# Performance work log

Hardware: AMD Instinct MI355X
Metric: run time of the kernel (lower is better)

Reference implementation:

```python
import jax, jax.numpy as jnp
import numpy as np

B, T, D = 2, 2048, 512
H = 8
DH = D // H
DECAY = 0.99
SCALE = DH ** -0.5
NEG = -1e30

_J6 = jnp.array([[0, 0, 0, 0, 0, 1], [0, 0, 0, 0, -1, 0], [0, 0, 0, 1, 0, 0],
                 [0, 0, 1, 0, 0, 0], [0, -1, 0, 0, 0, 0], [1, 0, 0, 0, 0, 0]],
                dtype=jnp.float32)
_PAIRS4 = [(0, 1), (0, 2), (0, 3), (1, 2), (1, 3), (2, 3)]


def exterior(p1, p2):
    # p1, p2: [..., 4] -> normalized Plucker line coords [..., 6]
    parts = [p1[..., i] * p2[..., j] - p1[..., j] * p2[..., i] for i, j in _PAIRS4]
    L = jnp.stack(parts, axis=-1)
    n = jnp.sqrt(jnp.sum(L * L, axis=-1, keepdims=True))
    return L / jnp.maximum(n, 1e-12)


def setup_inputs() -> dict:
    key = jax.random.key(0)
    ks = jax.random.split(key, 16)
    s = 0.02
    return {
        "x": jax.random.normal(ks[0], (B, T, D), jnp.float32),
        "qkv_w": jax.random.normal(ks[1], (3 * D, D), jnp.float32) * s,
        "qkv_b": jnp.zeros((3 * D,), jnp.float32),
        "w1_write": jax.random.normal(ks[2], (4 * H, D), jnp.float32) * s,
        "w2_write": jax.random.normal(ks[3], (4 * H, D), jnp.float32) * s,
        "w1_read": jax.random.normal(ks[4], (4 * H, D), jnp.float32) * s,
        "w2_read": jax.random.normal(ks[5], (4 * H, D), jnp.float32) * s,
        "mem_value_w": jax.random.normal(ks[6], (D, D), jnp.float32) * s,
        "mem_value_b": jnp.zeros((D,), jnp.float32),
        "mem_gate_w": jax.random.normal(ks[7], (H, D), jnp.float32) * s,
        "mem_gate_b": jnp.zeros((H,), jnp.float32),
        "mem_scale": jnp.full((H,), 0.1, jnp.float32),
        "out_w": jax.random.normal(ks[8], (D, D), jnp.float32) * s,
        "out_b": jnp.zeros((D,), jnp.float32),
    }


def reference(x, qkv_w, qkv_b, w1_write, w2_write, w1_read, w2_read,
              mem_value_w, mem_value_b, mem_gate_w, mem_gate_b, mem_scale,
              out_w, out_b):
    b, t, d = x.shape
    # --- standard causal attention (dropout in eval mode = identity) ---
    qkv = (x @ qkv_w.T + qkv_b).reshape(b, t, 3, H, DH)
    qkv = jnp.transpose(qkv, (2, 0, 3, 1, 4))  # [3,B,H,T,dh]
    q, k, v = qkv[0], qkv[1], qkv[2]
    scores = jnp.einsum('bhtd,bhsd->bhts', q, k) * SCALE
    i = jnp.arange(t)
    upper = i[:, None] < i[None, :]  # strictly upper -> masked
    scores = jnp.where(upper, NEG, scores)
    attn = jax.nn.softmax(scores, axis=-1)
    seq_out = jnp.einsum('bhts,bhsd->bhtd', attn, v)
    seq_out = jnp.transpose(seq_out, (0, 2, 1, 3)).reshape(b, t, d)
    # --- exterior-algebra Gram memory ---
    x_prev = jnp.concatenate([jnp.zeros((b, 1, d), x.dtype), x[:, :-1]], axis=1)
    w1 = (x_prev @ w1_write.T).reshape(b, t, H, 4)
    w2 = (x @ w2_write.T).reshape(b, t, H, 4)
    write_lines = exterior(w1, w2)  # [B,T,H,6]
    r1 = (x @ w1_read.T).reshape(b, t, H, 4)
    r2 = (x @ w2_read.T).reshape(b, t, H, 4)
    read_lines = exterior(r1, r2)  # [B,T,H,6]
    J_write = jnp.einsum('bthi,ij->bthj', write_lines, _J6)
    # incidence[b,h,i,j] = <read_i, J write_j>
    incidence = jnp.einsum('bihk,bjhk->bhij', read_lines, J_write)  # [B,H,T,T]
    # decay weights, strictly lower triangular (j < i); also acts as causal mask
    pos = jnp.arange(t, dtype=x.dtype)
    delta = pos[:, None] - pos[None, :]
    weights = jnp.where(delta > 0, jnp.power(jnp.asarray(DECAY, x.dtype), delta), 0.0)
    mem_score = jnp.sum((incidence * incidence) * weights[None, None], axis=-1)  # [B,H,T]
    # --- gating ---
    mem_val = x @ mem_value_w.T + mem_value_b  # [B,T,D]
    gate = jax.nn.sigmoid(x @ mem_gate_w.T + mem_gate_b)  # [B,T,H]
    mem_score_t = jnp.transpose(mem_score, (0, 2, 1))  # [B,T,H]
    gated = jax.nn.sigmoid(mem_score_t * mem_scale[None, None, :]) * gate
    gated = jnp.mean(gated, axis=-1, keepdims=True)  # [B,T,1]
    return (seq_out + gated * mem_val) @ out_w.T + out_b
```

## Files before the change

### kernel.cpp

```cpp
#include <hip/hip_runtime.h>
#include <math.h>

#define B_ 2
#define T_ 2048
#define D_ 512
#define H_ 8
#define DH_ 64
#define SCALE_ 0.125f
#define DECAY_ 0.99f

static constexpr size_t QSZ = (size_t)B_ * H_ * T_ * DH_;

typedef __bf16 bf16x8 __attribute__((ext_vector_type(8)));
typedef float f32x4 __attribute__((ext_vector_type(4)));

__device__ inline ushort f2bf(float f) {
  uint u = __float_as_uint(f);
  u += 0x7FFF + ((u >> 16) & 1);
  return (ushort)(u >> 16);
}

__device__ inline float bf2f(ushort v) {
  return __uint_as_float(((uint)v) << 16);
}

__device__ __forceinline__ void gload16(const ushort* g, ushort* l) {
  __builtin_amdgcn_global_load_lds(
      (const __attribute__((address_space(1))) void*)g,
      (__attribute__((address_space(3))) void*)l, 16, 0, 0);
}

__device__ __forceinline__ uint cvtpk(float lo, float hi) {
  uint r;
  asm("v_cvt_pk_bf16_f32 %0, %1, %2" : "=v"(r) : "v"(lo), "v"(hi));
  return r;
}

__global__ __launch_bounds__(256) void cast_bf16_kernel(
    const float* __restrict__ x, const float* __restrict__ qkvw,
    const float* __restrict__ mvw, const float* __restrict__ ow,
    const float* __restrict__ w1w, const float* __restrict__ w2w,
    const float* __restrict__ w1r, const float* __restrict__ w2r,
    const float* __restrict__ mgw, ushort* __restrict__ dst)
{
  size_t e0 = ((size_t)blockIdx.x * 256 + threadIdx.x) * 8;
  const float* src = nullptr;
  if (e0 < 2097152)      src = x + e0;
  else if (e0 < 2883584) src = qkvw + (e0 - 2097152);
  else if (e0 < 3145728) src = mvw + (e0 - 2883584);
  else if (e0 < 3276800) {
    size_t off = e0 - 3145728;
    int row = (int)(off >> 9), col = (int)(off & 511);
    if (row < 32)       src = w1w + (size_t)row * 512 + col;
    else if (row < 64)  src = w2w + (size_t)(row - 32) * 512 + col;
    else if (row < 96)  src = w1r + (size_t)(row - 64) * 512 + col;
    else if (row < 128) src = w2r + (size_t)(row - 96) * 512 + col;
    else if (row < 136) src = mgw + (size_t)(row - 128) * 512 + col;
    else src = nullptr;
  } else if (e0 < 3538944) src = ow + (e0 - 3276800);
  ushort tmp[8];
  if (src) {
    float4 a = *(const float4*)(src);
    float4 b = *(const float4*)(src + 4);
    tmp[0] = f2bf(a.x); tmp[1] = f2bf(a.y); tmp[2] = f2bf(a.z); tmp[3] = f2bf(a.w);
    tmp[4] = f2bf(b.x); tmp[5] = f2bf(b.y); tmp[6] = f2bf(b.z); tmp[7] = f2bf(b.w);
  } else {
#pragma unroll
    for (int i = 0; i < 8; i++) tmp[i] = 0;
  }
  *(uint4*)(dst + e0) = *(uint4*)tmp;
}

template<int EPI>
__global__ __launch_bounds__(256) void mfma_gemm(const ushort* __restrict__ A,
    const ushort* __restrict__ W, const float* __restrict__ bias,
    const float* __restrict__ bias2, void* __restrict__ Cout,
    ushort* __restrict__ memval16, float* __restrict__ proj, int M, int N, int K)
{
  __shared__ __align__(16) ushort As[128 * 64];
  __shared__ __align__(16) ushort Ws[64 * 64];
  const int tid = threadIdx.x;
  const int wave = tid >> 6, lane = tid & 63;
  const int col16 = lane & 15, grp = lane >> 4;
  const int wr = wave >> 1, wc = wave & 1;
  const int gx = gridDim.x;
  const int nwg = gx * gridDim.y;
  const int p = blockIdx.y * gx + blockIdx.x;
  const int wg = (p & 7) * (nwg >> 3) + (p >> 3);
  const int bm = (wg / gx) * 128, bn = (wg % gx) * 64;

  f32x4 acc[4][2] = {};
  const int lrow = lane >> 3, lcol = (lane & 7) * 8;

  for (int k0 = 0; k0 < K; k0 += 64) {
    __syncthreads();
#pragma unroll
    for (int i = 0; i < 4; i++) {
      int q = i * 4 + wave;
      gload16(A + (size_t)(bm + q * 8 + lrow) * K + k0 + lcol, &As[q * 512]);
    }
#pragma unroll
    for (int i = 0; i < 2; i++) {
      int q = i * 4 + wave;
      gload16(W + (size_t)(bn + q * 8 + lrow) * K + k0 + lcol, &Ws[q * 512]);
    }
    __syncthreads();
#pragma unroll
    for (int kk = 0; kk < 2; kk++) {
      bf16x8 a[4], b[2];
#pragma unroll
      for (int m = 0; m < 4; m++)
        a[m] = *(const bf16x8*)&As[(wr * 64 + m * 16 + col16) * 64 + kk * 32 + grp * 8];
#pragma unroll
      for (int n = 0; n < 2; n++)
        b[n] = *(const bf16x8*)&Ws[(wc * 32 + n * 16 + col16) * 64 + kk * 32 + grp * 8];
#pragma unroll
      for (int m = 0; m < 4; m++)
#pragma unroll
        for (int n = 0; n < 2; n++)
          acc[m][n] = __builtin_amdgcn_mfma_f32_16x16x32_bf16(a[m], b[n], acc[m][n], 0, 0, 0);
    }
  }

  if (EPI == 1) {
    ushort* q16 = (ushort*)Cout;
    ushort* k16 = q16 + QSZ;
    ushort* vt  = q16 + 2 * QSZ;
    const int sec = bn >> 9;
    if (sec == 2) {
#pragma unroll
      for (int n = 0; n < 2; n++) {
        int col = bn + wc * 32 + n * 16 + col16;
        float bv = bias[col];
        int h = (col >> 6) & 7, dh = col & 63;
#pragma unroll
        for (int m = 0; m < 4; m++) {
          int row0 = bm + wr * 64 + m * 16 + grp * 4;
          int b = row0 >> 11, t0 = row0 & 2047;
          int tq = (t0 & ~63) + ((t0 >> 5) & 1) * 32 + ((t0 >> 2) & 3) * 8
                 + ((t0 >> 4) & 1) * 4;
          ushort tmp4[4];
#pragma unroll
          for (int r = 0; r < 4; r++) tmp4[r] = f2bf(acc[m][n][r] + bv);
          *(uint2*)(vt + ((size_t)(b * H_ + h) * 64 + dh) * T_ + tq) = *(uint2*)tmp4;
        }
      }
    } else {
#pragma unroll
      for (int n = 0; n < 2; n++) {
        int col = bn + wc * 32 + n * 16 + col16;
        float bv;
        if (sec < 2)       bv = bias[col];
        else if (sec == 3) bv = bias2[col - 1536];
        else               bv = 0.f;
        int h = (col >> 6) & 7, dh = col & 63;
#pragma unroll
        for (int m = 0; m < 4; m++) {
#pragma unroll
          for (int r = 0; r < 4; r++) {
            int row = bm + wr * 64 + m * 16 + grp * 4 + r;
            int b = row >> 11, t = row & 2047;
            float val = acc[m][n][r] + bv;
            size_t bh = (size_t)(b * H_ + h);
            if (sec == 0)      q16[(bh * T_ + t) * 64 + dh] = f2bf(val * (SCALE_ * 1.44269504f));
            else if (sec == 1) k16[(bh * T_ + t) * 64 + dh] = f2bf(val);
            else if (sec == 3) memval16[(size_t)row * 512 + (col - 1536)] = f2bf(val);
            else               proj[(size_t)row * 256 + (col - 2048)] = val;
          }
        }
      }
    }
  } else {
    float* C = (float*)Cout;
#pragma unroll
    for (int n = 0; n < 2; n++) {
      int col = bn + wc * 32 + n * 16 + col16;
      float bv = bias[col];
#pragma unroll
      for (int m = 0; m < 4; m++) {
#pragma unroll
        for (int r = 0; r < 4; r++) {
          int row = bm + wr * 64 + m * 16 + grp * 4 + r;
          C[(size_t)row * N + col] = acc[m][n][r] + bv;
        }
      }
    }
  }
}

__global__ __launch_bounds__(256) void lines_kernel(
    const float* __restrict__ proj, const float* __restrict__ gb,
    float* __restrict__ u_out, float* __restrict__ r_out, float* __restrict__ gate_out)
{
  int gid = blockIdx.x * 256 + threadIdx.x;
  int bt = gid >> 3, h = gid & 7;
  int b = bt >> 11, t = bt & 2047;
  const float* pr = proj + (size_t)bt * 256;
  const int pi[6] = {0, 0, 0, 1, 1, 2};
  const int pj[6] = {1, 2, 3, 2, 3, 3};
  float p1[4], p2[4];
#pragma unroll
  for (int e = 0; e < 4; e++) {
    p1[e] = (t == 0) ? 0.f : proj[(size_t)(bt - 1) * 256 + h * 4 + e];
    p2[e] = pr[32 + h * 4 + e];
  }
  float L[6], n2 = 0.f;
#pragma unroll
  for (int e = 0; e < 6; e++) {
    L[e] = p1[pi[e]] * p2[pj[e]] - p1[pj[e]] * p2[pi[e]];
    n2 = fmaf(L[e], L[e], n2);
  }
  float inv = 1.f / fmaxf(sqrtf(n2), 1e-12f);
  size_t base = (((size_t)(b * H_ + h)) * T_ + t) * 6;
  u_out[base + 0] =  L[5] * inv;
  u_out[base + 1] = -L[4] * inv;
  u_out[base + 2] =  L[3] * inv;
  u_out[base + 3] =  L[2] * inv;
  u_out[base + 4] = -L[1] * inv;
  u_out[base + 5] =  L[0] * inv;
#pragma unroll
  for (int e = 0; e < 4; e++) {
    p1[e] = pr[64 + h * 4 + e];
    p2[e] = pr[96 + h * 4 + e];
  }
  n2 = 0.f;
#pragma unroll
  for (int e = 0; e < 6; e++) {
    L[e] = p1[pi[e]] * p2[pj[e]] - p1[pj[e]] * p2[pi[e]];
    n2 = fmaf(L[e], L[e], n2);
  }
  inv = 1.f / fmaxf(sqrtf(n2), 1e-12f);
#pragma unroll
  for (int e = 0; e < 6; e++) r_out[base + e] = L[e] * inv;
  gate_out[(size_t)bt * H_ + h] = 1.f / (1.f + __expf(-(pr[128 + h] + gb[h])));
}

__global__ __launch_bounds__(128) void memscore3_kernel(
    const float* __restrict__ u, const float* __restrict__ r, float* __restrict__ score)
{
  const int bh = blockIdx.x;
  const int c = blockIdx.y;
  const int tid = threadIdx.x;
  const int base = c << 7;
  const int jmax = base + 128;
  __shared__ float us_t[6][2048];
  __shared__ float red[128][25];

  const float* ug = u + (size_t)bh * T_ * 6;
  for (int idx = tid; idx < jmax * 6; idx += 128) {
    int j = idx / 6;
    int cmp = idx - j * 6;
    us_t[cmp][j] = ug[idx];
  }
  __syncthreads();

  float g[21];
#pragma unroll
  for (int q2 = 0; q2 < 21; q2++) g[q2] = 0.f;
  if (c > 0) {
    float w = __powf(DECAY_, (float)(128 - tid));
    const float d128 = 0.27624712f;
    for (int j = base - 128 + tid; j >= 0; j -= 128) {
      float u0 = us_t[0][j], u1 = us_t[1][j], u2 = us_t[2][j];
      float u3 = us_t[3][j], u4 = us_t[4][j], u5 = us_t[5][j];
      float w0 = w * u0, w1 = w * u1, w2 = w * u2, w3 = w * u3, w4 = w * u4;
      g[0] = fmaf(w0, u0, g[0]);  g[1] = fmaf(w0, u1, g[1]);
      g[2] = fmaf(w0, u2, g[2]);  g[3] = fmaf(w0, u3, g[3]);
      g[4] = fmaf(w0, u4, g[4]);  g[5] = fmaf(w0, u5, g[5]);
      g[6] = fmaf(w1, u1, g[6]);  g[7] = fmaf(w1, u2, g[7]);
      g[8] = fmaf(w1, u3, g[8]);  g[9] = fmaf(w1, u4, g[9]);
      g[10] = fmaf(w1, u5, g[10]); g[11] = fmaf(w2, u2, g[11]);
      g[12] = fmaf(w2, u3, g[12]); g[13] = fmaf(w2, u4, g[13]);
      g[14] = fmaf(w2, u5, g[14]); g[15] = fmaf(w3, u3, g[15]);
      g[16] = fmaf(w3, u4, g[16]); g[17] = fmaf(w3, u5, g[17]);
      g[18] = fmaf(w4, u4, g[18]); g[19] = fmaf(w4, u5, g[19]);
      g[20] = fmaf(w * u5, u5, g[20]);
      w *= d128;
    }
  }
#pragma unroll
  for (int q2 = 0; q2 < 21; q2++) red[tid][q2] = g[q2];
  __syncthreads();
  for (int off = 64; off > 0; off >>= 1) {
    if (tid < off) {
#pragma unroll
      for (int q2 = 0; q2 < 21; q2++) red[tid][q2] += red[tid + off][q2];
    }
    __syncthreads();
  }
  float M21[21];
#pragma unroll
  for (int q2 = 0; q2 < 21; q2++) M21[q2] = red[0][q2];

  const int i = base + tid;
  const float* ri = r + ((size_t)bh * T_ + i) * 6;
  float r0 = ri[0], r1 = ri[1], r2 = ri[2], r3 = ri[3], r4 = ri[4], r5 = ri[5];
  float q = M21[0] * r0 * r0 + M21[6] * r1 * r1 + M21[11] * r2 * r2
          + M21[15] * r3 * r3 + M21[18] * r4 * r4 + M21[20] * r5 * r5
          + 2.f * (M21[1] * r0 * r1 + M21[2] * r0 * r2 + M21[3] * r0 * r3
                 + M21[4] * r0 * r4 + M21[5] * r0 * r5 + M21[7] * r1 * r2
                 + M21[8] * r1 * r3 + M21[9] * r1 * r4 + M21[10] * r1 * r5
                 + M21[12] * r2 * r3 + M21[13] * r2 * r4 + M21[14] * r2 * r5
                 + M21[16] * r3 * r4 + M21[17] * r3 * r5 + M21[19] * r4 * r5);
  float wl = __powf(DECAY_, (float)tid);
  float sum = q * wl;
  float w = wl;
  const float invd = 1.0f / DECAY_;
  const int sbound = tid | 63;
  for (int s = 0; s < sbound; ++s) {
    float d = r0 * us_t[0][base + s] + r1 * us_t[1][base + s]
            + r2 * us_t[2][base + s] + r3 * us_t[3][base + s]
            + r4 * us_t[4][base + s] + r5 * us_t[5][base + s];
    if (s < tid) sum = fmaf(w, d * d, sum);
    w *= invd;
  }
  score[(size_t)bh * T_ + i] = sum;
}

__global__ __launch_bounds__(256) void gfac_kernel(
    const float* __restrict__ score, const float* __restrict__ gate,
    const float* __restrict__ mem_scale, float* __restrict__ gfac)
{
  int bt = blockIdx.x * 256 + threadIdx.x;
  int b = bt >> 11, t = bt & 2047;
  float acc = 0.f;
#pragma unroll
  for (int h = 0; h < H_; h++) {
    float ms = score[((size_t)(b * H_ + h)) * T_ + t];
    float sg = 1.f / (1.f + __expf(-ms * mem_scale[h]));
    acc += sg * gate[(size_t)bt * H_ + h];
  }
  gfac[bt] = acc * (1.0f / H_);
}

__global__ __launch_bounds__(256) void attn_v4_kernel(
    const ushort* __restrict__ q16, const ushort* __restrict__ k16,
    const ushort* __restrict__ vtp16, const ushort* __restrict__ memval16,
    const float* __restrict__ gfac, ushort* __restrict__ seqo16)
{
  const int blk = blockIdx.x;
  const int bh = blk & 15;
  const int rg = 63 - (blk >> 4);
  const int tid = threadIdx.x;
  const int w = tid >> 6, lane = tid & 63;
  const int col16 = lane & 15, grp = lane >> 4;

  __shared__ __align__(16) float comb[3][64][40];

  const int i0 = rg * 32;
  const ushort* qp0 = q16 + ((size_t)bh * T_ + i0 + col16) * 64 + grp * 8;
  bf16x8 aq[2][2];
  aq[0][0] = *(const bf16x8*)(qp0);
  aq[0][1] = *(const bf16x8*)(qp0 + 32);
  aq[1][0] = *(const bf16x8*)(qp0 + 16 * 64);
  aq[1][1] = *(const bf16x8*)(qp0 + 16 * 64 + 32);

  f32x4 ot[2][4] = {};
  float lsum[2] = {0.f, 0.f};

  const ushort* kb = k16 + (size_t)bh * T_ * 64;
  const ushort* vb = vtp16 + (size_t)bh * 64 * T_;

  const int ntiles = (rg >> 1) + 1;
  for (int kt = w; kt < ntiles; kt += 4) {
    const int j0 = kt * 64;
    bf16x8 vf[2][4];
#pragma unroll
    for (int ks = 0; ks < 2; ks++)
#pragma unroll
      for (int n4 = 0; n4 < 4; n4++)
        vf[ks][n4] = *(const bf16x8*)(vb + (size_t)(n4 * 16 + col16) * T_ +
                                      j0 + ks * 32 + grp * 8);
    const bool lastt = (kt == ntiles - 1);
    uint pk[2][4][2];
#pragma unroll
    for (int jt = 0; jt < 4; jt++) {
      const ushort* kp = kb + (size_t)(j0 + jt * 16 + col16) * 64 + grp * 8;
      bf16x8 b0 = *(const bf16x8*)kp;
      bf16x8 b1 = *(const bf16x8*)(kp + 32);
#pragma unroll
      for (int rr = 0; rr < 2; rr++) {
        f32x4 facc = {};
        facc = __builtin_amdgcn_mfma_f32_16x16x32_bf16(b0, aq[rr][0], facc, 0, 0, 0);
        facc = __builtin_amdgcn_mfma_f32_16x16x32_bf16(b1, aq[rr][1], facc, 0, 0, 0);
        const int i = i0 + rr * 16 + col16;
        float p[4];
#pragma unroll
        for (int r = 0; r < 4; r++) {
          int j = j0 + jt * 16 + grp * 4 + r;
          p[r] = (lastt && j > i) ? 0.f : exp2f(facc[r]);
          lsum[rr] += p[r];
        }
        pk[rr][jt][0] = cvtpk(p[0], p[1]);
        pk[rr][jt][1] = cvtpk(p[2], p[3]);
      }
    }
#pragma unroll
    for (int ks = 0; ks < 2; ks++)
#pragma unroll
      for (int rr = 0; rr < 2; rr++) {
        uint pf_u[4] = {pk[rr][2 * ks][0], pk[rr][2 * ks][1],
                        pk[rr][2 * ks + 1][0], pk[rr][2 * ks + 1][1]};
        bf16x8 pf = *(bf16x8*)pf_u;
#pragma unroll
        for (int n4 = 0; n4 < 4; n4++)
          ot[rr][n4] = __builtin_amdgcn_mfma_f32_16x16x32_bf16(vf[ks][n4], pf, ot[rr][n4], 0, 0, 0);
      }
  }

#pragma unroll
  for (int rr = 0; rr < 2; rr++) {
    lsum[rr] += __shfl_xor(lsum[rr], 16);
    lsum[rr] += __shfl_xor(lsum[rr], 32);
  }

  if (w > 0) {
    float* dst = &comb[w - 1][lane][0];
#pragma unroll
    for (int rr = 0; rr < 2; rr++)
#pragma unroll
      for (int n4 = 0; n4 < 4; n4++)
        *(float4*)&dst[(rr * 4 + n4) * 4] = *(float4*)&ot[rr][n4];
    dst[32] = lsum[0];
    dst[33] = lsum[1];
  }
  __syncthreads();
  if (w == 0) {
#pragma unroll
    for (int ww = 0; ww < 3; ww++) {
      const float* src = &comb[ww][lane][0];
#pragma unroll
      for (int rr = 0; rr < 2; rr++)
#pragma unroll
        for (int n4 = 0; n4 < 4; n4++) {
          float4 v = *(const float4*)&src[(rr * 4 + n4) * 4];
          ot[rr][n4][0] += v.x; ot[rr][n4][1] += v.y;
          ot[rr][n4][2] += v.z; ot[rr][n4][3] += v.w;
        }
      lsum[0] += src[32];
      lsum[1] += src[33];
    }
    const int b = bh >> 3, h = bh & 7;
#pragma unroll
    for (int rr = 0; rr < 2; rr++) {
      const int i = i0 + rr * 16 + col16;
      const float inv = 1.f / lsum[rr];
      const float gf = gfac[b * T_ + i];
      const size_t rowbase = ((size_t)(b * T_) + i) * D_ + h * 64 + grp * 4;
#pragma unroll
      for (int n4 = 0; n4 < 4; n4++) {
        ushort tmp4[4];
#pragma unroll
        for (int r = 0; r < 4; r++) {
          float mv = bf2f(memval16[rowbase + n4 * 16 + r]);
          tmp4[r] = f2bf(fmaf(gf, mv, ot[rr][n4][r] * inv));
        }
        *(uint2*)(seqo16 + rowbase + n4 * 16) = *(uint2*)tmp4;
      }
    }
  }
}

extern "C" void kernel_launch(void* const* d_in, const int* in_sizes, int n_in,
                              void* d_out, int out_size, void* d_ws, size_t ws_size,
                              hipStream_t stream) {
  const float* x     = (const float*)d_in[0];
  const float* qkvw  = (const float*)d_in[1];
  const float* qkvb  = (const float*)d_in[2];
  const float* w1w   = (const float*)d_in[3];
  const float* w2w   = (const float*)d_in[4];
  const float* w1r   = (const float*)d_in[5];
  const float* w2r   = (const float*)d_in[6];
  const float* mvw   = (const float*)d_in[7];
  const float* mvb   = (const float*)d_in[8];
  const float* mgw   = (const float*)d_in[9];
  const float* mgb   = (const float*)d_in[10];
  const float* mscl  = (const float*)d_in[11];
  const float* ow    = (const float*)d_in[12];
  const float* ob    = (const float*)d_in[13];
  (void)in_sizes; (void)n_in; (void)out_size; (void)ws_size;

  float* f = (float*)d_ws;
  float* proj   = f;
  float* ul     = proj + 1048576;
  float* rl     = ul + 196608;
  float* gatep  = rl + 196608;
  float* msc    = gatep + 32768;
  float* gfac   = msc + 32768;
  ushort* x16    = (ushort*)(gfac + 4096);
  ushort* wbig16 = x16 + 2097152;
  ushort* ow16   = wbig16 + 1179648;
  ushort* q16    = ow16 + 262144;
  ushort* k16    = q16 + QSZ;
  ushort* vt16   = k16 + QSZ;
  ushort* memval16 = vt16 + QSZ;
  ushort* seqo16 = x16;

  const int M = B_ * T_;

  cast_bf16_kernel<<<dim3(1728), 256, 0, stream>>>(x, qkvw, mvw, ow,
                                                   w1w, w2w, w1r, w2r, mgw, x16);
  mfma_gemm<1><<<dim3(36, 32), 256, 0, stream>>>(x16, wbig16, qkvb, mvb, q16,
                                                 memval16, proj, M, 2304, D_);
  lines_kernel<<<dim3(128), 256, 0, stream>>>(proj, mgb, ul, rl, gatep);
  memscore3_kernel<<<dim3(16, 16), 128, 0, stream>>>(ul, rl, msc);
  gfac_kernel<<<dim3(16), 256, 0, stream>>>(msc, gatep, mscl, gfac);
  attn_v4_kernel<<<dim3(16 * 64), 256, 0, stream>>>(q16, k16, vt16, memval16,
                                                    gfac, seqo16);
  mfma_gemm<0><<<dim3(8, 32), 256, 0, stream>>>(seqo16, ow16, ob, nullptr, d_out,
                                                nullptr, nullptr, M, D_, D_);
}
```

Before: 111.3 us.

## Prefetch next K/V tile into registers and map heads to XCDs in attention

The attention kernel now loads the next K and V fragments into registers while computing on the current tile, a software double buffer meant to hide global-memory latency. Block indices are also remapped so each XCD handles two fixed batch-head pairs, keeping each head's K/V inside one XCD's L2. The cost is more live registers, which may lower occupancy or cause spills.

```diff
diff --git a/kernel.cpp b/kernel.cpp
--- a/kernel.cpp
+++ b/kernel.cpp
@@ -333,14 +333,15 @@
   gfac[bt] = acc * (1.0f / H_);
 }
 
-__global__ __launch_bounds__(256) void attn_v4_kernel(
+__global__ __launch_bounds__(256) void attn_v5_kernel(
     const ushort* __restrict__ q16, const ushort* __restrict__ k16,
     const ushort* __restrict__ vtp16, const ushort* __restrict__ memval16,
     const float* __restrict__ gfac, ushort* __restrict__ seqo16)
 {
   const int blk = blockIdx.x;
-  const int bh = blk & 15;
-  const int rg = 63 - (blk >> 4);
+  const int xcd = blk & 7, rank = blk >> 3;
+  const int bh = (xcd << 1) | (rank & 1);
+  const int rg = 63 - (rank >> 1);
   const int tid = threadIdx.x;
   const int w = tid >> 6, lane = tid & 63;
   const int col16 = lane & 15, grp = lane >> 4;
@@ -362,27 +363,53 @@
   const ushort* vb = vtp16 + (size_t)bh * 64 * T_;
 
   const int ntiles = (rg >> 1) + 1;
-  for (int kt = w; kt < ntiles; kt += 4) {
+
+  bf16x8 k0f[4], k1f[4], vf[2][4];
+  int kt = w;
+  if (kt < ntiles) {
     const int j0 = kt * 64;
-    bf16x8 vf[2][4];
+#pragma unroll
+    for (int jt = 0; jt < 4; jt++) {
+      const ushort* kp = kb + (size_t)(j0 + jt * 16 + col16) * 64 + grp * 8;
+      k0f[jt] = *(const bf16x8*)kp;
+      k1f[jt] = *(const bf16x8*)(kp + 32);
+    }
 #pragma unroll
     for (int ks = 0; ks < 2; ks++)
 #pragma unroll
       for (int n4 = 0; n4 < 4; n4++)
         vf[ks][n4] = *(const bf16x8*)(vb + (size_t)(n4 * 16 + col16) * T_ +
                                       j0 + ks * 32 + grp * 8);
+  }
+
+  for (; kt < ntiles; kt += 4) {
+    const int j0 = kt * 64;
+    const bool more = (kt + 4) < ntiles;
+    bf16x8 nk0[4], nk1[4], nv[2][4];
+    if (more) {
+      const int jn = (kt + 4) * 64;
+#pragma unroll
+      for (int jt = 0; jt < 4; jt++) {
+        const ushort* kp = kb + (size_t)(jn + jt * 16 + col16) * 64 + grp * 8;
+        nk0[jt] = *(const bf16x8*)kp;
+        nk1[jt] = *(const bf16x8*)(kp + 32);
+      }
+#pragma unroll
+      for (int ks = 0; ks < 2; ks++)
+#pragma unroll
+        for (int n4 = 0; n4 < 4; n4++)
+          nv[ks][n4] = *(const bf16x8*)(vb + (size_t)(n4 * 16 + col16) * T_ +
+                                        jn + ks * 32 + grp * 8);
+    }
     const bool lastt = (kt == ntiles - 1);
     uint pk[2][4][2];
 #pragma unroll
     for (int jt = 0; jt < 4; jt++) {
-      const ushort* kp = kb + (size_t)(j0 + jt * 16 + col16) * 64 + grp * 8;
-      bf16x8 b0 = *(const bf16x8*)kp;
-      bf16x8 b1 = *(const bf16x8*)(kp + 32);
 #pragma unroll
       for (int rr = 0; rr < 2; rr++) {
         f32x4 facc = {};
-        facc = __builtin_amdgcn_mfma_f32_16x16x32_bf16(b0, aq[rr][0], facc, 0, 0, 0);
-        facc = __builtin_amdgcn_mfma_f32_16x16x32_bf16(b1, aq[rr][1], facc, 0, 0, 0);
+        facc = __builtin_amdgcn_mfma_f32_16x16x32_bf16(k0f[jt], aq[rr][0], facc, 0, 0, 0);
+        facc = __builtin_amdgcn_mfma_f32_16x16x32_bf16(k1f[jt], aq[rr][1], facc, 0, 0, 0);
         const int i = i0 + rr * 16 + col16;
         float p[4];
 #pragma unroll
@@ -406,6 +433,14 @@
         for (int n4 = 0; n4 < 4; n4++)
           ot[rr][n4] = __builtin_amdgcn_mfma_f32_16x16x32_bf16(vf[ks][n4], pf, ot[rr][n4], 0, 0, 0);
       }
+    if (more) {
+#pragma unroll
+      for (int jt = 0; jt < 4; jt++) { k0f[jt] = nk0[jt]; k1f[jt] = nk1[jt]; }
+#pragma unroll
+      for (int ks = 0; ks < 2; ks++)
+#pragma unroll
+        for (int n4 = 0; n4 < 4; n4++) vf[ks][n4] = nv[ks][n4];
+    }
   }
 
 #pragma unroll
@@ -505,7 +540,7 @@
   lines_kernel<<<dim3(128), 256, 0, stream>>>(proj, mgb, ul, rl, gatep);
   memscore3_kernel<<<dim3(16, 16), 128, 0, stream>>>(ul, rl, msc);
   gfac_kernel<<<dim3(16), 256, 0, stream>>>(msc, gatep, mscl, gfac);
-  attn_v4_kernel<<<dim3(16 * 64), 256, 0, stream>>>(q16, k16, vt16, memval16,
+  attn_v5_kernel<<<dim3(16 * 64), 256, 0, stream>>>(q16, k16, vt16, memval16,
                                                     gfac, seqo16);
   mfma_gemm<0><<<dim3(8, 32), 256, 0, stream>>>(seqo16, ow16, ob, nullptr, d_out,
                                                 nullptr, nullptr, M, D_, D_);
```

Result: no change. 111.0 us (-0.2%).

## Double attention query tile to 64 rows per block to reuse K/V loads

Applied to the files above, without the earlier changes.

Each attention block now handles 64 query rows instead of 32, so every K and V tile loaded from global memory feeds four 16-row MFMA groups instead of two, and the grid is halved. The V fragment loads and P packing are restructured per 32-column half to keep register pressure manageable, and the cross-wave reduction buffer is enlarged. The trade-off is higher VGPR use and fewer blocks, which lowers occupancy and gives coarser load balance over the causal triangle.

```diff
diff --git a/kernel.cpp b/kernel.cpp
--- a/kernel.cpp
+++ b/kernel.cpp
@@ -333,83 +333,83 @@
   gfac[bt] = acc * (1.0f / H_);
 }
 
-__global__ __launch_bounds__(256) void attn_v4_kernel(
+__global__ __launch_bounds__(256) void attn_v6_kernel(
     const ushort* __restrict__ q16, const ushort* __restrict__ k16,
     const ushort* __restrict__ vtp16, const ushort* __restrict__ memval16,
     const float* __restrict__ gfac, ushort* __restrict__ seqo16)
 {
   const int blk = blockIdx.x;
   const int bh = blk & 15;
-  const int rg = 63 - (blk >> 4);
+  const int rg = 31 - (blk >> 4);
   const int tid = threadIdx.x;
   const int w = tid >> 6, lane = tid & 63;
   const int col16 = lane & 15, grp = lane >> 4;
 
-  __shared__ __align__(16) float comb[3][64][40];
-
-  const int i0 = rg * 32;
+  __shared__ __align__(16) float comb[3][64][68];
+
+  const int i0 = rg * 64;
   const ushort* qp0 = q16 + ((size_t)bh * T_ + i0 + col16) * 64 + grp * 8;
-  bf16x8 aq[2][2];
-  aq[0][0] = *(const bf16x8*)(qp0);
-  aq[0][1] = *(const bf16x8*)(qp0 + 32);
-  aq[1][0] = *(const bf16x8*)(qp0 + 16 * 64);
-  aq[1][1] = *(const bf16x8*)(qp0 + 16 * 64 + 32);
-
-  f32x4 ot[2][4] = {};
-  float lsum[2] = {0.f, 0.f};
+  bf16x8 aq[4][2];
+#pragma unroll
+  for (int rr = 0; rr < 4; rr++) {
+    aq[rr][0] = *(const bf16x8*)(qp0 + rr * 16 * 64);
+    aq[rr][1] = *(const bf16x8*)(qp0 + rr * 16 * 64 + 32);
+  }
+
+  f32x4 ot[4][4] = {};
+  float lsum[4] = {0.f, 0.f, 0.f, 0.f};
 
   const ushort* kb = k16 + (size_t)bh * T_ * 64;
   const ushort* vb = vtp16 + (size_t)bh * 64 * T_;
 
-  const int ntiles = (rg >> 1) + 1;
+  const int ntiles = rg + 1;
   for (int kt = w; kt < ntiles; kt += 4) {
     const int j0 = kt * 64;
-    bf16x8 vf[2][4];
-#pragma unroll
-    for (int ks = 0; ks < 2; ks++)
+    const bool lastt = (kt == ntiles - 1);
+#pragma unroll
+    for (int ks = 0; ks < 2; ks++) {
+      bf16x8 vf[4];
 #pragma unroll
       for (int n4 = 0; n4 < 4; n4++)
-        vf[ks][n4] = *(const bf16x8*)(vb + (size_t)(n4 * 16 + col16) * T_ +
-                                      j0 + ks * 32 + grp * 8);
-    const bool lastt = (kt == ntiles - 1);
-    uint pk[2][4][2];
-#pragma unroll
-    for (int jt = 0; jt < 4; jt++) {
-      const ushort* kp = kb + (size_t)(j0 + jt * 16 + col16) * 64 + grp * 8;
-      bf16x8 b0 = *(const bf16x8*)kp;
-      bf16x8 b1 = *(const bf16x8*)(kp + 32);
-#pragma unroll
-      for (int rr = 0; rr < 2; rr++) {
-        f32x4 facc = {};
-        facc = __builtin_amdgcn_mfma_f32_16x16x32_bf16(b0, aq[rr][0], facc, 0, 0, 0);
-        facc = __builtin_amdgcn_mfma_f32_16x16x32_bf16(b1, aq[rr][1], facc, 0, 0, 0);
-        const int i = i0 + rr * 16 + col16;
-        float p[4];
-#pragma unroll
-        for (int r = 0; r < 4; r++) {
-          int j = j0 + jt * 16 + grp * 4 + r;
-          p[r] = (lastt && j > i) ? 0.f : exp2f(facc[r]);
-          lsum[rr] += p[r];
+        vf[n4] = *(const bf16x8*)(vb + (size_t)(n4 * 16 + col16) * T_ +
+                                  j0 + ks * 32 + grp * 8);
+      uint pk[4][2][2];
+#pragma unroll
+      for (int jtl = 0; jtl < 2; jtl++) {
+        const int jt = ks * 2 + jtl;
+        const ushort* kp = kb + (size_t)(j0 + jt * 16 + col16) * 64 + grp * 8;
+        bf16x8 b0 = *(const bf16x8*)kp;
+        bf16x8 b1 = *(const bf16x8*)(kp + 32);
+#pragma unroll
+        for (int rr = 0; rr < 4; rr++) {
+          f32x4 facc = {};
+          facc = __builtin_amdgcn_mfma_f32_16x16x32_bf16(b0, aq[rr][0], facc, 0, 0, 0);
+          facc = __builtin_amdgcn_mfma_f32_16x16x32_bf16(b1, aq[rr][1], facc, 0, 0, 0);
+          const int i = i0 + rr * 16 + col16;
+          float p[4];
+#pragma unroll
+          for (int r = 0; r < 4; r++) {
+            int j = j0 + jt * 16 + grp * 4 + r;
+            p[r] = (lastt && j > i) ? 0.f : exp2f(facc[r]);
+            lsum[rr] += p[r];
+          }
+          pk[rr][jtl][0] = cvtpk(p[0], p[1]);
+          pk[rr][jtl][1] = cvtpk(p[2], p[3]);
         }
-        pk[rr][jt][0] = cvtpk(p[0], p[1]);
-        pk[rr][jt][1] = cvtpk(p[2], p[3]);
       }
-    }
-#pragma unroll
-    for (int ks = 0; ks < 2; ks++)
-#pragma unroll
-      for (int rr = 0; rr < 2; rr++) {
-        uint pf_u[4] = {pk[rr][2 * ks][0], pk[rr][2 * ks][1],
-                        pk[rr][2 * ks + 1][0], pk[rr][2 * ks + 1][1]};
+#pragma unroll
+      for (int rr = 0; rr < 4; rr++) {
+        uint pf_u[4] = {pk[rr][0][0], pk[rr][0][1], pk[rr][1][0], pk[rr][1][1]};
         bf16x8 pf = *(bf16x8*)pf_u;
 #pragma unroll
         for (int n4 = 0; n4 < 4; n4++)
-          ot[rr][n4] = __builtin_amdgcn_mfma_f32_16x16x32_bf16(vf[ks][n4], pf, ot[rr][n4], 0, 0, 0);
+          ot[rr][n4] = __builtin_amdgcn_mfma_f32_16x16x32_bf16(vf[n4], pf, ot[rr][n4], 0, 0, 0);
       }
-  }
-
-#pragma unroll
-  for (int rr = 0; rr < 2; rr++) {
+    }
+  }
+
+#pragma unroll
+  for (int rr = 0; rr < 4; rr++) {
     lsum[rr] += __shfl_xor(lsum[rr], 16);
     lsum[rr] += __shfl_xor(lsum[rr], 32);
   }
@@ -417,12 +417,11 @@
   if (w > 0) {
     float* dst = &comb[w - 1][lane][0];
 #pragma unroll
-    for (int rr = 0; rr < 2; rr++)
+    for (int rr = 0; rr < 4; rr++)
 #pragma unroll
       for (int n4 = 0; n4 < 4; n4++)
         *(float4*)&dst[(rr * 4 + n4) * 4] = *(float4*)&ot[rr][n4];
-    dst[32] = lsum[0];
-    dst[33] = lsum[1];
+    *(float4*)&dst[64] = make_float4(lsum[0], lsum[1], lsum[2], lsum[3]);
   }
   __syncthreads();
   if (w == 0) {
@@ -430,19 +429,19 @@
     for (int ww = 0; ww < 3; ww++) {
       const float* src = &comb[ww][lane][0];
 #pragma unroll
-      for (int rr = 0; rr < 2; rr++)
+      for (int rr = 0; rr < 4; rr++)
 #pragma unroll
         for (int n4 = 0; n4 < 4; n4++) {
           float4 v = *(const float4*)&src[(rr * 4 + n4) * 4];
           ot[rr][n4][0] += v.x; ot[rr][n4][1] += v.y;
           ot[rr][n4][2] += v.z; ot[rr][n4][3] += v.w;
         }
-      lsum[0] += src[32];
-      lsum[1] += src[33];
+      float4 lv = *(const float4*)&src[64];
+      lsum[0] += lv.x; lsum[1] += lv.y; lsum[2] += lv.z; lsum[3] += lv.w;
     }
     const int b = bh >> 3, h = bh & 7;
 #pragma unroll
-    for (int rr = 0; rr < 2; rr++) {
+    for (int rr = 0; rr < 4; rr++) {
       const int i = i0 + rr * 16 + col16;
       const float inv = 1.f / lsum[rr];
       const float gf = gfac[b * T_ + i];
@@ -505,7 +504,7 @@
   lines_kernel<<<dim3(128), 256, 0, stream>>>(proj, mgb, ul, rl, gatep);
   memscore3_kernel<<<dim3(16, 16), 128, 0, stream>>>(ul, rl, msc);
   gfac_kernel<<<dim3(16), 256, 0, stream>>>(msc, gatep, mscl, gfac);
-  attn_v4_kernel<<<dim3(16 * 64), 256, 0, stream>>>(q16, k16, vt16, memval16,
+  attn_v6_kernel<<<dim3(16 * 32), 256, 0, stream>>>(q16, k16, vt16, memval16,
                                                     gfac, seqo16);
   mfma_gemm<0><<<dim3(8, 32), 256, 0, stream>>>(seqo16, ow16, ob, nullptr, d_out,
                                                 nullptr, nullptr, M, D_, D_);
```

Measured after the change: 110.0 us. About the same (-1.1%).
